# Kernel optimization log

Hardware: AMD Instinct MI355X
Metric: run time of the kernel (lower is better)

## Reference

```python
import jax, jax.numpy as jnp
import numpy as np

CROP = 3          # crop_size
MAX_CROP = 2 * CROP  # 6 -> 6x6 = 36 offsets (faithful to range(max_crop))
H = 384


def reference(predict, target, target_mask):
    # mask both images
    t = target * target_mask
    p = predict * target_mask

    B, C, _, _ = p.shape
    hw = H - MAX_CROP  # 378

    # cropped target: [:, :, 3:-3, 3:-3] -> [B, C, 378, 378]
    ct = t[:, :, CROP:-CROP, CROP:-CROP]

    def c_mse_at(u, v):
        # shifted predict window [B, C, 378, 378]
        cp = jax.lax.dynamic_slice(p, (0, 0, u, v), (B, C, hw, hw))
        bb = jnp.mean(ct - cp)           # brightness bias (scalar)
        return jnp.mean((cp + bb - ct) ** 2)  # MSE after bias correction

    offs = jnp.arange(MAX_CROP)
    uu, vv = jnp.meshgrid(offs, offs, indexing='ij')
    losses = jax.vmap(c_mse_at)(uu.ravel(), vv.ravel())  # [36]

    cMSE = jnp.min(losses)
    score = -10.0 * jnp.log10(cMSE)  # cPSNR
    return score


def setup_inputs() -> dict:
    key = jax.random.key(0)
    k1, k2, k3 = jax.random.split(key, 3)
    shape = (32, 1, 384, 384)
    predict = jax.random.uniform(k1, shape, dtype=jnp.float32)
    target = jax.random.uniform(k2, shape, dtype=jnp.float32)
    target_mask = jax.random.uniform(k3, shape, dtype=jnp.float32)
    return {"predict": predict, "target": target, "target_mask": target_mask}
```

## Files before the change

### kernel.cpp

```cpp
#include <hip/hip_runtime.h>
#include <hip/hip_bf16.h>
#include <math.h>


#define NIMG 32
#define IMGSZ (384 * 384)
#define NRT 126
#define NSG 48
#define BSZ 128
#define NCC 1512
#define NEDGE 64
#define NTOT (NCC + NEDGE)
#define CHUNK 197
#define NM 40
#define MSTRIDE 1512
#define MQUADS 378
#define NE 262

__global__ __launch_bounds__(BSZ) void probav_fused_kernel(
    const float* __restrict__ predict,
    const float* __restrict__ target,
    const float* __restrict__ mask,
    float* __restrict__ mpart ,
    double* __restrict__ epart ) {

  const int lbid = (blockIdx.x & 7) * CHUNK + (blockIdx.x >> 3);

  __shared__ double shbuf[506];
  const int t = threadIdx.x;
  const int lane = t & 63;
  const int w = t >> 6;

  if (lbid >= NEDGE) {
    const int cb  = lbid - NEDGE;
    const int tid = cb * BSZ + t;
    const int img = tid / (NRT * NSG);
    const int rem = tid - img * (NRT * NSG);
    const int rt  = rem / NSG;
    const int sg  = rem - rt * NSG;
    const int r0  = rt * 3;
    const int jb  = sg * 8;
    const size_t base = (size_t)img * IMGSZ;

    float ct[3][8];
    float t1 = 0.f, t2 = 0.f;
#pragma unroll
    for (int rr = 0; rr < 3; ++rr) {
      const float4* tq = reinterpret_cast<const float4*>(target + base + (size_t)(r0 + rr + 3) * 384 + jb);
      const float4* mq = reinterpret_cast<const float4*>(mask   + base + (size_t)(r0 + rr + 3) * 384 + jb);
      float tv[12], mv[12];
#pragma unroll
      for (int q = 0; q < 3; ++q) {
        float4 a = tq[q];
        float4 b = mq[q];
        tv[4 * q + 0] = a.x; tv[4 * q + 1] = a.y; tv[4 * q + 2] = a.z; tv[4 * q + 3] = a.w;
        mv[4 * q + 0] = b.x; mv[4 * q + 1] = b.y; mv[4 * q + 2] = b.z; mv[4 * q + 3] = b.w;
      }
#pragma unroll
      for (int x = 0; x < 8; ++x) {
        float v = tv[3 + x] * mv[3 + x];
        v = (jb + x < 378) ? v : 0.f;
        ct[rr][x] = v;
        t1 += v;
        t2 = fmaf(v, v, t2);
      }
    }

    float cc[36];
#pragma unroll
    for (int o = 0; o < 36; ++o) cc[o] = 0.f;
    float tot1 = 0.f, tot2 = 0.f;
    const int ownR = (rt == NRT - 1) ? 8 : 3;

#pragma unroll
    for (int R = 0; R < 8; ++R) {
      const float4* pq = reinterpret_cast<const float4*>(predict + base + (size_t)(r0 + R) * 384 + jb);
      const float4* mq = reinterpret_cast<const float4*>(mask    + base + (size_t)(r0 + R) * 384 + jb);
      float pm[16];
#pragma unroll
      for (int q = 0; q < 4; ++q) {
        float4 a = pq[q];
        float4 b = mq[q];
        pm[4 * q + 0] = a.x * b.x;
        pm[4 * q + 1] = a.y * b.y;
        pm[4 * q + 2] = a.z * b.z;
        pm[4 * q + 3] = a.w * b.w;
      }
      if (R < ownR) {
#pragma unroll
        for (int x = 0; x < 8; ++x) {
          tot1 += pm[x];
          tot2 = fmaf(pm[x], pm[x], tot2);
        }
      }
      const int rlo = (R > 5) ? (R - 5) : 0;
      const int rhi = (R < 2) ? R : 2;
#pragma unroll
      for (int rr = rlo; rr <= rhi; ++rr) {
        const int u = R - rr;
#pragma unroll
        for (int v = 0; v < 6; ++v) {
#pragma unroll
          for (int x = 0; x < 8; ++x) {
            cc[u * 6 + v] = fmaf(ct[rr][x], pm[v + x], cc[u * 6 + v]);
          }
        }
      }
    }

    float* red = reinterpret_cast<float*>(shbuf);
#pragma unroll
    for (int o = 0; o < 36; ++o) {
      float a = cc[o];
#pragma unroll
      for (int off = 32; off > 0; off >>= 1) a += __shfl_down(a, off);
      if (lane == 0) red[w * NM + o] = a;
    }
    {
      float a = t1, b = t2, c = tot1, d = tot2;
#pragma unroll
      for (int off = 32; off > 0; off >>= 1) {
        a += __shfl_down(a, off);
        b += __shfl_down(b, off);
        c += __shfl_down(c, off);
        d += __shfl_down(d, off);
      }
      if (lane == 0) { red[w * NM + 36] = a; red[w * NM + 37] = b; red[w * NM + 38] = c; red[w * NM + 39] = d; }
    }
    __syncthreads();
    if (t < NM) {
      mpart[t * MSTRIDE + cb] = red[0 * NM + t] + red[1 * NM + t];
    }
  } else {
    const int img = lbid >> 1;
    const int slice = lbid & 1;
    const size_t base = (size_t)img * IMGSZ;
    double* sh = shbuf;

    if (slice == 0) {
      if (t < 120) {
        const int ridx = t / 12, cs = t % 12;
        const int row = (ridx < 5) ? ridx : (373 + ridx);
        const float* pr = predict + base + (size_t)row * 384;
        const float* mr = mask    + base + (size_t)row * 384;
        double e1 = 0.0, e2 = 0.0;
        for (int c = cs; c < 384; c += 12) {
          float v = pr[c] * mr[c];
          e1 += v;
          e2 += (double)v * v;
        }
        sh[ridx * 12 + cs] = e1;
        sh[120 + ridx * 12 + cs] = e2;
      }
      __syncthreads();
      if (t < 20) {
        const int kind = t / 10, ridx = t % 10;
        double s = 0.0;
        for (int k = 0; k < 12; ++k) s += sh[kind * 120 + ridx * 12 + k];
        epart[(size_t)(kind * 10 + ridx) * NIMG + img] = s;
      }
      if (t < 110) {
        const int ridx = t / 11, cidx = t % 11;
        const int row = (ridx < 5) ? ridx : (373 + ridx);
        const int col = (cidx < 5) ? cidx : (373 + cidx);
        float v = predict[base + (size_t)row * 384 + col] * mask[base + (size_t)row * 384 + col];
        epart[(size_t)(42 + t)  * NIMG + img] = (double)v;
        epart[(size_t)(152 + t) * NIMG + img] = (double)v * v;
      }
    } else {
      if (t < 121) {
        const int cidx = t / 11, rs = t % 11;
        const int col = (cidx < 5) ? cidx : (373 + cidx);
        double f1 = 0.0, f2 = 0.0;
        for (int r = rs; r < 383; r += 11) {
          float v = predict[base + (size_t)r * 384 + col] * mask[base + (size_t)r * 384 + col];
          f1 += v;
          f2 += (double)v * v;
        }
        sh[cidx * 11 + rs] = f1;
        sh[121 + cidx * 11 + rs] = f2;
      }
      __syncthreads();
      if (t < 22) {
        const int kind = t / 11, cidx = t % 11;
        double s = 0.0;
        for (int k = 0; k < 11; ++k) s += sh[kind * 121 + cidx * 11 + k];
        epart[(size_t)(20 + kind * 11 + cidx) * NIMG + img] = s;
      }
    }
  }
}

__global__ void probav_final_kernel(const float* __restrict__ mpart,
                                    const double* __restrict__ epart,
                                    float* __restrict__ out) {
  __shared__ double M[NM];
  __shared__ double E[NE];
  __shared__ double Etmp[524];
  __shared__ double loss[36];
  const int t = threadIdx.x;
  const int lane = t & 63;
  const int w = t >> 6;

  for (int v = w; v < NM; v += 16) {
    const float4* qp = reinterpret_cast<const float4*>(mpart + v * MSTRIDE);
    double s = 0.0;
    for (int i = lane; i < MQUADS; i += 64) {
      float4 q = qp[i];
      s += (double)q.x + (double)q.y + (double)q.z + (double)q.w;
    }
#pragma unroll
    for (int off = 32; off > 0; off >>= 1) s += __shfl_down(s, off);
    if (lane == 0) M[v] = s;
  }
  if (t < 524) {
    const int e = t >> 1, si = t & 1;
    double s = 0.0;
    for (int i = si * 16; i < si * 16 + 16; ++i) s += epart[(size_t)e * NIMG + i];
    Etmp[t] = s;
  }
  __syncthreads();
  if (t < NE) E[t] = Etmp[2 * t] + Etmp[2 * t + 1];
  __syncthreads();

  if (t < 36) {
    const int u = t / 6, v = t % 6;
    double br1 = 0, br2 = 0, bc1 = 0, bc2 = 0, x1 = 0, x2 = 0;
    int rset[5], nr = 0;
    for (int j = 0; j < u; ++j) rset[nr++] = j;
    for (int j = 5 + u; j < 10; ++j) rset[nr++] = j;
    int cset[6], nc = 0;
    for (int j = 0; j < v; ++j) cset[nc++] = j;
    for (int j = 5 + v; j < 11; ++j) cset[nc++] = j;
    for (int a = 0; a < nr; ++a) { br1 += E[rset[a]]; br2 += E[10 + rset[a]]; }
    for (int b = 0; b < nc; ++b) { bc1 += E[20 + cset[b]]; bc2 += E[31 + cset[b]]; }
    for (int a = 0; a < nr; ++a)
      for (int b = 0; b < nc; ++b) {
        x1 += E[42 + rset[a] * 11 + cset[b]];
        x2 += E[152 + rset[a] * 11 + cset[b]];
      }
    const double T1 = M[36], T2 = M[37];
    const double W1 = M[38] - br1 - bc1 + x1;
    const double W2 = M[39] - br2 - bc2 + x2;
    const double CCv = M[t];
    const double N = 32.0 * 378.0 * 378.0;
    const double S1 = T1 - W1;
    const double S2 = T2 - 2.0 * CCv + W2;
    loss[t] = S2 / N - (S1 / N) * (S1 / N);
  }
  __syncthreads();
  if (t == 0) {
    double best = loss[0];
    for (int o = 1; o < 36; ++o) best = fmin(best, loss[o]);
    out[0] = (float)(-10.0 * log10(best));
  }
}

extern "C" void kernel_launch(void* const* d_in, const int* in_sizes, int n_in,
                              void* d_out, int out_size, void* d_ws, size_t ws_size,
                              hipStream_t stream) {
  const float* predict = (const float*)d_in[0];
  const float* target  = (const float*)d_in[1];
  const float* mask    = (const float*)d_in[2];
  float* out = (float*)d_out;

  float*  mpart = (float*)d_ws;
  double* epart = (double*)((char*)d_ws + NM * MSTRIDE * 4);

  probav_fused_kernel<<<NTOT, BSZ, 0, stream>>>(predict, target, mask, mpart, epart);
  probav_final_kernel<<<1, 1024, 0, stream>>>(mpart, epart, out);
}
```

Measured before the change: 52.95 us.

## Widen per-thread column tile to 16 and use wave-shuffle edge reductions

Each correlation thread now covers 16 output columns instead of 8, halving the number of column groups and blocks. This cuts the redundant halo loads of predict and mask, since 24 floats are loaded per row for 16 outputs instead of 16 for 8, and raises the FMA work per load. The edge blocks now reduce row and column sums with wave shuffles instead of shared memory plus __syncthreads, and the block swizzle is recomputed with padding and an early return. In exchange, per-thread register pressure grows (48 ct values, 21 pm values, 36 accumulators), which may lower occupancy or cause spills.

```diff
diff --git a/kernel.cpp b/kernel.cpp
--- a/kernel.cpp
+++ b/kernel.cpp
@@ -6,15 +6,15 @@
 #define NIMG 32
 #define IMGSZ (384 * 384)
 #define NRT 126
-#define NSG 48
+#define NSG 24
 #define BSZ 128
-#define NCC 1512
+#define NCC 756
 #define NEDGE 64
-#define NTOT (NCC + NEDGE)
-#define CHUNK 197
+#define CCPAD 760
+#define CHUNK 95
 #define NM 40
-#define MSTRIDE 1512
-#define MQUADS 378
+#define MSTRIDE 756
+#define MQUADS 189
 #define NE 262
 
 __global__ __launch_bounds__(BSZ) void probav_fused_kernel(
@@ -24,40 +24,50 @@
     float* __restrict__ mpart ,
     double* __restrict__ epart ) {
 
-  const int lbid = (blockIdx.x & 7) * CHUNK + (blockIdx.x >> 3);
-
-  __shared__ double shbuf[506];
   const int t = threadIdx.x;
   const int lane = t & 63;
   const int w = t >> 6;
 
-  if (lbid >= NEDGE) {
-    const int cb  = lbid - NEDGE;
+  if (blockIdx.x >= NEDGE) {
+    const int i = blockIdx.x - NEDGE;
+    const int cb = (i & 7) * CHUNK + (i >> 3);
+    if (cb >= NCC) return;
+
+    __shared__ float red[2 * NM];
+
     const int tid = cb * BSZ + t;
     const int img = tid / (NRT * NSG);
     const int rem = tid - img * (NRT * NSG);
     const int rt  = rem / NSG;
     const int sg  = rem - rt * NSG;
     const int r0  = rt * 3;
-    const int jb  = sg * 8;
+    const int jb  = sg * 16;
     const size_t base = (size_t)img * IMGSZ;
-
-    float ct[3][8];
+    const bool isLastRt = (rt == NRT - 1);
+
+    int qc[6];
+#pragma unroll
+    for (int q = 0; q < 6; ++q) {
+      int c = jb + 4 * q;
+      qc[q] = (c > 380) ? 380 : c;
+    }
+
+    float ct[3][16];
     float t1 = 0.f, t2 = 0.f;
 #pragma unroll
     for (int rr = 0; rr < 3; ++rr) {
-      const float4* tq = reinterpret_cast<const float4*>(target + base + (size_t)(r0 + rr + 3) * 384 + jb);
-      const float4* mq = reinterpret_cast<const float4*>(mask   + base + (size_t)(r0 + rr + 3) * 384 + jb);
-      float tv[12], mv[12];
-#pragma unroll
-      for (int q = 0; q < 3; ++q) {
-        float4 a = tq[q];
-        float4 b = mq[q];
+      const float* trow = target + base + (size_t)(r0 + rr + 3) * 384;
+      const float* mrow = mask   + base + (size_t)(r0 + rr + 3) * 384;
+      float tv[20], mv[20];
+#pragma unroll
+      for (int q = 0; q < 5; ++q) {
+        float4 a = *reinterpret_cast<const float4*>(trow + qc[q]);
+        float4 b = *reinterpret_cast<const float4*>(mrow + qc[q]);
         tv[4 * q + 0] = a.x; tv[4 * q + 1] = a.y; tv[4 * q + 2] = a.z; tv[4 * q + 3] = a.w;
         mv[4 * q + 0] = b.x; mv[4 * q + 1] = b.y; mv[4 * q + 2] = b.z; mv[4 * q + 3] = b.w;
       }
 #pragma unroll
-      for (int x = 0; x < 8; ++x) {
+      for (int x = 0; x < 16; ++x) {
         float v = tv[3 + x] * mv[3 + x];
         v = (jb + x < 378) ? v : 0.f;
         ct[rr][x] = v;
@@ -70,25 +80,25 @@
 #pragma unroll
     for (int o = 0; o < 36; ++o) cc[o] = 0.f;
     float tot1 = 0.f, tot2 = 0.f;
-    const int ownR = (rt == NRT - 1) ? 8 : 3;
+    const int ownR = isLastRt ? 8 : 3;
 
 #pragma unroll
     for (int R = 0; R < 8; ++R) {
-      const float4* pq = reinterpret_cast<const float4*>(predict + base + (size_t)(r0 + R) * 384 + jb);
-      const float4* mq = reinterpret_cast<const float4*>(mask    + base + (size_t)(r0 + R) * 384 + jb);
-      float pm[16];
-#pragma unroll
-      for (int q = 0; q < 4; ++q) {
-        float4 a = pq[q];
-        float4 b = mq[q];
-        pm[4 * q + 0] = a.x * b.x;
-        pm[4 * q + 1] = a.y * b.y;
-        pm[4 * q + 2] = a.z * b.z;
-        pm[4 * q + 3] = a.w * b.w;
+      const float* prow = predict + base + (size_t)(r0 + R) * 384;
+      const float* mrow = mask    + base + (size_t)(r0 + R) * 384;
+      float pm[21];
+#pragma unroll
+      for (int q = 0; q < 6; ++q) {
+        float4 a = *reinterpret_cast<const float4*>(prow + qc[q]);
+        float4 b = *reinterpret_cast<const float4*>(mrow + qc[q]);
+        if (4 * q + 0 < 21) pm[4 * q + 0] = a.x * b.x;
+        if (4 * q + 1 < 21) pm[4 * q + 1] = a.y * b.y;
+        if (4 * q + 2 < 21) pm[4 * q + 2] = a.z * b.z;
+        if (4 * q + 3 < 21) pm[4 * q + 3] = a.w * b.w;
       }
       if (R < ownR) {
 #pragma unroll
-        for (int x = 0; x < 8; ++x) {
+        for (int x = 0; x < 16; ++x) {
           tot1 += pm[x];
           tot2 = fmaf(pm[x], pm[x], tot2);
         }
@@ -101,14 +111,13 @@
 #pragma unroll
         for (int v = 0; v < 6; ++v) {
 #pragma unroll
-          for (int x = 0; x < 8; ++x) {
+          for (int x = 0; x < 16; ++x) {
             cc[u * 6 + v] = fmaf(ct[rr][x], pm[v + x], cc[u * 6 + v]);
           }
         }
       }
     }
 
-    float* red = reinterpret_cast<float*>(shbuf);
 #pragma unroll
     for (int o = 0; o < 36; ++o) {
       float a = cc[o];
@@ -132,32 +141,31 @@
       mpart[t * MSTRIDE + cb] = red[0 * NM + t] + red[1 * NM + t];
     }
   } else {
-    const int img = lbid >> 1;
-    const int slice = lbid & 1;
+    const int img = blockIdx.x >> 1;
+    const int slice = blockIdx.x & 1;
     const size_t base = (size_t)img * IMGSZ;
-    double* sh = shbuf;
 
     if (slice == 0) {
-      if (t < 120) {
-        const int ridx = t / 12, cs = t % 12;
+      for (int ridx = w; ridx < 10; ridx += 2) {
         const int row = (ridx < 5) ? ridx : (373 + ridx);
         const float* pr = predict + base + (size_t)row * 384;
         const float* mr = mask    + base + (size_t)row * 384;
         double e1 = 0.0, e2 = 0.0;
-        for (int c = cs; c < 384; c += 12) {
-          float v = pr[c] * mr[c];
+#pragma unroll
+        for (int k = 0; k < 6; ++k) {
+          float v = pr[lane + 64 * k] * mr[lane + 64 * k];
           e1 += v;
           e2 += (double)v * v;
         }
-        sh[ridx * 12 + cs] = e1;
-        sh[120 + ridx * 12 + cs] = e2;
-      }
-      __syncthreads();
-      if (t < 20) {
-        const int kind = t / 10, ridx = t % 10;
-        double s = 0.0;
-        for (int k = 0; k < 12; ++k) s += sh[kind * 120 + ridx * 12 + k];
-        epart[(size_t)(kind * 10 + ridx) * NIMG + img] = s;
+#pragma unroll
+        for (int off = 32; off > 0; off >>= 1) {
+          e1 += __shfl_down(e1, off);
+          e2 += __shfl_down(e2, off);
+        }
+        if (lane == 0) {
+          epart[(size_t)ridx        * NIMG + img] = e1;
+          epart[(size_t)(10 + ridx) * NIMG + img] = e2;
+        }
       }
       if (t < 110) {
         const int ridx = t / 11, cidx = t % 11;
@@ -168,24 +176,27 @@
         epart[(size_t)(152 + t) * NIMG + img] = (double)v * v;
       }
     } else {
-      if (t < 121) {
-        const int cidx = t / 11, rs = t % 11;
+      for (int cidx = w; cidx < 11; cidx += 2) {
         const int col = (cidx < 5) ? cidx : (373 + cidx);
         double f1 = 0.0, f2 = 0.0;
-        for (int r = rs; r < 383; r += 11) {
-          float v = predict[base + (size_t)r * 384 + col] * mask[base + (size_t)r * 384 + col];
-          f1 += v;
-          f2 += (double)v * v;
-        }
-        sh[cidx * 11 + rs] = f1;
-        sh[121 + cidx * 11 + rs] = f2;
-      }
-      __syncthreads();
-      if (t < 22) {
-        const int kind = t / 11, cidx = t % 11;
-        double s = 0.0;
-        for (int k = 0; k < 11; ++k) s += sh[kind * 121 + cidx * 11 + k];
-        epart[(size_t)(20 + kind * 11 + cidx) * NIMG + img] = s;
+#pragma unroll
+        for (int k = 0; k < 6; ++k) {
+          const int r = lane + 64 * k;
+          if (r < 383) {
+            float v = predict[base + (size_t)r * 384 + col] * mask[base + (size_t)r * 384 + col];
+            f1 += v;
+            f2 += (double)v * v;
+          }
+        }
+#pragma unroll
+        for (int off = 32; off > 0; off >>= 1) {
+          f1 += __shfl_down(f1, off);
+          f2 += __shfl_down(f2, off);
+        }
+        if (lane == 0) {
+          epart[(size_t)(20 + cidx) * NIMG + img] = f1;
+          epart[(size_t)(31 + cidx) * NIMG + img] = f2;
+        }
       }
     }
   }
@@ -267,6 +278,6 @@
   float*  mpart = (float*)d_ws;
   double* epart = (double*)((char*)d_ws + NM * MSTRIDE * 4);
 
-  probav_fused_kernel<<<NTOT, BSZ, 0, stream>>>(predict, target, mask, mpart, epart);
+  probav_fused_kernel<<<NEDGE + CCPAD, BSZ, 0, stream>>>(predict, target, mask, mpart, epart);
   probav_final_kernel<<<1, 1024, 0, stream>>>(mpart, epart, out);
 }
```

New measurement: 61.37 us, median of 2. 1.16x slower.
